# Optimization experiments

Measured on AMD Instinct MI355X. Metric: run time of the kernel, lower is better.

Reference implementation:

```python
import jax, jax.numpy as jnp
import numpy as np

B, S, D = 2, 2048, 2048
H, DK, DV, LD = 16, 128, 128, 64


def setup_inputs() -> dict:
    key = jax.random.key(0)
    ks = jax.random.split(key, 12)
    s = lambda fan_in: 1.0 / np.sqrt(fan_in)
    return {
        "queries": jax.random.normal(ks[0], (B, S, D), jnp.float32),
        "keys": jax.random.normal(ks[1], (B, S, D), jnp.float32),
        "values": jax.random.normal(ks[2], (B, S, D), jnp.float32),
        # linear_q: Linear(D, DK*H)
        "Wq": jax.random.uniform(ks[3], (D, DK * H), jnp.float32, -s(D), s(D)),
        "bq": jax.random.uniform(ks[4], (DK * H,), jnp.float32, -s(D), s(D)),
        # latent_k_proj / latent_v_proj: Linear(D, LD*H)
        "Wlk": jax.random.uniform(ks[5], (D, LD * H), jnp.float32, -s(D), s(D)),
        "blk": jax.random.uniform(ks[6], (LD * H,), jnp.float32, -s(D), s(D)),
        "Wlv": jax.random.uniform(ks[7], (D, LD * H), jnp.float32, -s(D), s(D)),
        "blv": jax.random.uniform(ks[8], (LD * H,), jnp.float32, -s(D), s(D)),
        # k/v reconstruction: Linear(LD, DK/DV, bias=False), stored [LD, DK]
        "Wkr": jax.random.uniform(ks[9], (LD, DK), jnp.float32, -s(LD), s(LD)),
        "Wvr": jax.random.uniform(ks[10], (LD, DV), jnp.float32, -s(LD), s(LD)),
        # linear_out: Linear(DV*H, D)
        "Wout": jax.random.uniform(ks[11], (DV * H, D), jnp.float32, -s(DV * H), s(DV * H)),
        "bout": jnp.zeros((D,), jnp.float32),
    }


def reference(queries, keys, values, Wq, bq, Wlk, blk, Wlv, blv, Wkr, Wvr, Wout, bout):
    b, sq, _ = queries.shape
    sk = keys.shape[1]
    # Q projection -> [b, H, sq, DK]
    q = (queries @ Wq + bq).reshape(b, sq, H, DK).transpose(0, 2, 1, 3)
    # Low-rank latent K/V -> [b, H, sk, LD]
    lk = (keys @ Wlk + blk).reshape(b, sk, H, LD).transpose(0, 2, 1, 3)
    lv = (values @ Wlv + blv).reshape(b, sk, H, LD).transpose(0, 2, 1, 3)
    # Reconstruct full K/V from latents -> [b, H, sk, DK/DV]
    k = lk @ Wkr
    v = lv @ Wvr
    scores = jnp.einsum('bhqd,bhkd->bhqk', q, k) / np.sqrt(DK).astype(np.float32)
    causal = jnp.triu(jnp.ones((sq, sk), dtype=bool), k=1)
    scores = jnp.where(causal, -jnp.inf, scores)
    attn = jax.nn.softmax(scores, axis=-1)
    out = jnp.einsum('bhqk,bhkd->bhqd', attn, v)  # [b, H, sq, DV]
    out = out.transpose(0, 2, 1, 3).reshape(b, sq, H * DV)
    return out @ Wout + bout
```

## Files before the change

kernel.cpp:

```cpp
#include <hip/hip_runtime.h>

#define S_LEN 2048
#define NH 16

typedef unsigned short u16;
typedef __attribute__((ext_vector_type(8))) short bf16x8;
typedef __attribute__((ext_vector_type(4))) short s16x4;
typedef __attribute__((ext_vector_type(4))) unsigned short u16x4;
typedef __attribute__((ext_vector_type(4))) unsigned int u32x4;
typedef __attribute__((ext_vector_type(4))) float f32x4;

__device__ __forceinline__ u16 f2bf(float f) {
  union { float f; unsigned int i; } x; x.f = f;
  unsigned int r = x.i + 0x7FFFu + ((x.i >> 16) & 1u);
  return (u16)(r >> 16);
}
__device__ __forceinline__ unsigned pk2(float lo, float hi) {
  unsigned r;
  asm("v_cvt_pk_bf16_f32 %0, %1, %2" : "=v"(r) : "v"(lo), "v"(hi));
  return r;
}
__device__ __forceinline__ void glds16(const void* g, void* l) {
  __builtin_amdgcn_global_load_lds((const __attribute__((address_space(1))) void*)g,
                                   (__attribute__((address_space(3))) void*)l, 16, 0, 0);
}

__global__ __launch_bounds__(256) void cast_f32_bf16(const float* __restrict__ in,
                                                     u16* __restrict__ out) {
  size_t i = ((size_t)blockIdx.x * 256 + threadIdx.x) * 8;
  f32x4 a = *(const f32x4*)&in[i];
  f32x4 b = *(const f32x4*)&in[i + 4];
  u32x4 o;
  o[0] = pk2(a[0], a[1]);
  o[1] = pk2(a[2], a[3]);
  o[2] = pk2(b[0], b[1]);
  o[3] = pk2(b[2], b[3]);
  *(u32x4*)&out[i] = o;
}

__global__ __launch_bounds__(256) void cast2_f32_bf16(const float* __restrict__ i0,
                                                      const float* __restrict__ i1,
                                                      u16* __restrict__ o0,
                                                      u16* __restrict__ o1) {
  const float* in = blockIdx.y ? i1 : i0;
  u16* out = blockIdx.y ? o1 : o0;
  size_t i = ((size_t)blockIdx.x * 256 + threadIdx.x) * 8;
  f32x4 a = *(const f32x4*)&in[i];
  f32x4 b = *(const f32x4*)&in[i + 4];
  u32x4 o;
  o[0] = pk2(a[0], a[1]);
  o[1] = pk2(a[2], a[3]);
  o[2] = pk2(b[0], b[1]);
  o[3] = pk2(b[2], b[3]);
  *(u32x4*)&out[i] = o;
}

__global__ __launch_bounds__(256) void transpose2_f32_bf16(const float* __restrict__ i0,
                                                           const float* __restrict__ i1,
                                                           u16* __restrict__ o0,
                                                           u16* __restrict__ o1,
                                                           int K, int N) {
  const float* in = blockIdx.z ? i1 : i0;
  u16* out = blockIdx.z ? o1 : o0;
  __shared__ u16 tile[64][72];
  int k0 = blockIdx.y * 64, n0 = blockIdx.x * 64;
  int t = threadIdx.x;
#pragma unroll
  for (int i = 0; i < 4; ++i) {
    int idx = i * 256 + t;
    int r = idx >> 4;
    int c4 = (idx & 15) << 2;
    f32x4 v = *(const f32x4*)&in[(size_t)(k0 + r) * N + n0 + c4];
#pragma unroll
    for (int j = 0; j < 4; ++j) tile[r][c4 + j] = f2bf(v[j]);
  }
  __syncthreads();
#pragma unroll
  for (int i = 0; i < 4; ++i) {
    int idx = i * 256 + t;
    int r = idx >> 4;
    int c4 = (idx & 15) << 2;
    u16x4 v;
    v[0] = tile[c4 + 0][r];
    v[1] = tile[c4 + 1][r];
    v[2] = tile[c4 + 2][r];
    v[3] = tile[c4 + 3][r];
    *(u16x4*)&out[(size_t)(n0 + r) * K + k0 + c4] = v;
  }
}

__global__ __launch_bounds__(256) void transpose_f32_bf16(const float* __restrict__ in,
                                                          u16* __restrict__ out,
                                                          int K, int N) {
  __shared__ u16 tile[64][72];
  int k0 = blockIdx.y * 64, n0 = blockIdx.x * 64;
  int t = threadIdx.x;
#pragma unroll
  for (int i = 0; i < 4; ++i) {
    int idx = i * 256 + t;
    int r = idx >> 4;
    int c4 = (idx & 15) << 2;
    f32x4 v = *(const f32x4*)&in[(size_t)(k0 + r) * N + n0 + c4];
#pragma unroll
    for (int j = 0; j < 4; ++j) tile[r][c4 + j] = f2bf(v[j]);
  }
  __syncthreads();
#pragma unroll
  for (int i = 0; i < 4; ++i) {
    int idx = i * 256 + t;
    int r = idx >> 4;
    int c4 = (idx & 15) << 2;
    u16x4 v;
    v[0] = tile[c4 + 0][r];
    v[1] = tile[c4 + 1][r];
    v[2] = tile[c4 + 2][r];
    v[3] = tile[c4 + 3][r];
    *(u16x4*)&out[(size_t)(n0 + r) * K + k0 + c4] = v;
  }
}

__global__ __launch_bounds__(256) void absorb_q(const u16* __restrict__ Wkr,
                                                const u16* __restrict__ Wqb,
                                                u16* __restrict__ Wq2T) {
  int kb = blockIdx.x, h = blockIdx.y;
  int t = threadIdx.x, w = t >> 6, lane = t & 63, lq = lane & 15, hi = lane >> 4;
  int k0 = kb * 128 + w * 32;
  f32x4 acc[4][2];
#pragma unroll
  for (int i = 0; i < 4; ++i)
#pragma unroll
    for (int j = 0; j < 2; ++j) acc[i][j] = (f32x4){0.f, 0.f, 0.f, 0.f};
#pragma unroll
  for (int kk = 0; kk < 4; ++kk) {
    bf16x8 a[4], bb[2];
#pragma unroll
    for (int fld = 0; fld < 4; ++fld)
      a[fld] = *(const bf16x8*)&Wkr[(fld * 16 + lq) * 128 + kk * 32 + hi * 8];
#pragma unroll
    for (int fk = 0; fk < 2; ++fk)
      bb[fk] = *(const bf16x8*)&Wqb[(size_t)(k0 + fk * 16 + lq) * 2048 + h * 128 + kk * 32 + hi * 8];
#pragma unroll
    for (int fld = 0; fld < 4; ++fld)
#pragma unroll
      for (int fk = 0; fk < 2; ++fk)
        acc[fld][fk] = __builtin_amdgcn_mfma_f32_16x16x32_bf16(a[fld], bb[fk], acc[fld][fk], 0, 0, 0);
  }
#pragma unroll
  for (int fld = 0; fld < 4; ++fld)
#pragma unroll
    for (int fk = 0; fk < 2; ++fk)
#pragma unroll
      for (int r = 0; r < 4; ++r)
        Wq2T[(size_t)(h * 64 + fld * 16 + hi * 4 + r) * 2048 + k0 + fk * 16 + lq] =
            f2bf(acc[fld][fk][r]);
}

__global__ __launch_bounds__(256) void absorb_o(const u16* __restrict__ WoutT,
                                                const u16* __restrict__ Wvr,
                                                u16* __restrict__ W2T) {
  int nb = blockIdx.x, h = blockIdx.y;
  int t = threadIdx.x, w = t >> 6, lane = t & 63, lq = lane & 15, hi = lane >> 4;
  int n0 = nb * 128 + w * 32;
  f32x4 acc[2][4];
#pragma unroll
  for (int i = 0; i < 2; ++i)
#pragma unroll
    for (int j = 0; j < 4; ++j) acc[i][j] = (f32x4){0.f, 0.f, 0.f, 0.f};
#pragma unroll
  for (int kk = 0; kk < 4; ++kk) {
    bf16x8 a[2], bb[4];
#pragma unroll
    for (int fn = 0; fn < 2; ++fn)
      a[fn] = *(const bf16x8*)&WoutT[(size_t)(n0 + fn * 16 + lq) * 2048 + h * 128 + kk * 32 + hi * 8];
#pragma unroll
    for (int fld = 0; fld < 4; ++fld)
      bb[fld] = *(const bf16x8*)&Wvr[(fld * 16 + lq) * 128 + kk * 32 + hi * 8];
#pragma unroll
    for (int fn = 0; fn < 2; ++fn)
#pragma unroll
      for (int fld = 0; fld < 4; ++fld)
        acc[fn][fld] = __builtin_amdgcn_mfma_f32_16x16x32_bf16(a[fn], bb[fld], acc[fn][fld], 0, 0, 0);
  }
#pragma unroll
  for (int fn = 0; fn < 2; ++fn)
#pragma unroll
    for (int fld = 0; fld < 4; ++fld)
#pragma unroll
      for (int r = 0; r < 4; ++r)
        W2T[(size_t)(n0 + fn * 16 + hi * 4 + r) * 1024 + h * 64 + fld * 16 + lq] =
            f2bf(acc[fn][fld][r]);
}

__global__ __launch_bounds__(256) void absorb_bq(const float* __restrict__ bq,
                                                 const float* __restrict__ Wkr,
                                                 float* __restrict__ bq2) {
  int n = blockIdx.x * 256 + threadIdx.x;
  int h = n >> 6, ld = n & 63;
  float s = 0.f;
#pragma unroll 8
  for (int dk = 0; dk < 128; ++dk) s += bq[h * 128 + dk] * Wkr[ld * 128 + dk];
  bq2[n] = s;
}

__global__ __launch_bounds__(256, 3) void gemm_projf(const float* __restrict__ A0,
                                                     const float* __restrict__ A1,
                                                     const float* __restrict__ A2,
                                                     const u16* __restrict__ W0,
                                                     const u16* __restrict__ W1,
                                                     const u16* __restrict__ W2,
                                                     const float* __restrict__ b0,
                                                     const float* __restrict__ b1,
                                                     const float* __restrict__ b2,
                                                     u16* __restrict__ C0,
                                                     u16* __restrict__ C1,
                                                     u16* __restrict__ C2) {
  const int N = 1024, K = 2048, nxl = 3, NT = 64;
  __shared__ u16 abuf[2][128 * 32];
  __shared__ u16 bbuf[3][128 * 32];

  int Lb = blockIdx.x;
  int xcd = Lb & 7, slot = Lb >> 3;
  int panel = ((slot >> nxl) << 3) + xcd;
  int x = slot & ((1 << nxl) - 1);
  int z = panel >> 5, y = panel & 31;

  const float* A = z == 0 ? A0 : (z == 1 ? A1 : A2);
  const u16* Wt = z == 0 ? W0 : (z == 1 ? W1 : W2);
  const float* bias = z == 0 ? b0 : (z == 1 ? b1 : b2);
  u16* C = z == 0 ? C0 : (z == 1 ? C1 : C2);

  int m0 = y * 128, n0 = x * 128;
  int t = threadIdx.x;
  int lane = t & 63, lq = lane & 15, hi = lane >> 4;
  int w = t >> 6, wm = w >> 1, wn = w & 1;

  struct a16 { f32x4 lo, hi; };
  a16 areg[2][2];

  f32x4 acc[4][4];
#pragma unroll
  for (int im = 0; im < 4; ++im)
#pragma unroll
    for (int fn = 0; fn < 4; ++fn) acc[im][fn] = (f32x4){0.f, 0.f, 0.f, 0.f};

#define LOADA(SLOT, KT)                                                              \
  do {                                                                               \
    int kb_ = (KT) * 32;                                                             \
    _Pragma("unroll") for (int i = 0; i < 2; ++i) {                                  \
      int idx = i * 256 + t, row = idx >> 2, c = idx & 3;                            \
      const float* ap = &A[(size_t)(m0 + row) * K + kb_ + ((c ^ ((row >> 1) & 3)) << 3)]; \
      areg[SLOT][i].lo = *(const f32x4*)ap;                                          \
      areg[SLOT][i].hi = *(const f32x4*)(ap + 4);                                    \
    }                                                                                \
  } while (0)

#define WRITEA(SLOT)                                                                 \
  do {                                                                               \
    _Pragma("unroll") for (int i = 0; i < 2; ++i) {                                  \
      u32x4 o;                                                                       \
      o[0] = pk2(areg[SLOT][i].lo[0], areg[SLOT][i].lo[1]);                          \
      o[1] = pk2(areg[SLOT][i].lo[2], areg[SLOT][i].lo[3]);                          \
      o[2] = pk2(areg[SLOT][i].hi[0], areg[SLOT][i].hi[1]);                          \
      o[3] = pk2(areg[SLOT][i].hi[2], areg[SLOT][i].hi[3]);                          \
      *(u32x4*)&abuf[SLOT][(i * 256 + t) * 8] = o;                                   \
    }                                                                                \
  } while (0)

#define STAGEB(KT)                                                                   \
  do {                                                                               \
    int kb_ = (KT) * 32;                                                             \
    u16* lB_ = &bbuf[(KT) % 3][0];                                                   \
    _Pragma("unroll") for (int i = 0; i < 2; ++i) {                                  \
      int idx = i * 256 + t, row = idx >> 2, c = idx & 3;                            \
      glds16(&Wt[(size_t)(n0 + row) * K + kb_ + ((c ^ ((row >> 1) & 3)) << 3)], lB_ + idx * 8); \
    }                                                                                \
  } while (0)

#define COMPUTE(PAR, TT)                                                             \
  do {                                                                               \
    const u16* lB_ = &bbuf[(TT) % 3][0];                                             \
    bf16x8 bf[4];                                                                    \
    _Pragma("unroll") for (int fn = 0; fn < 4; ++fn) {                               \
      int row = wn * 64 + fn * 16 + lq;                                              \
      bf[fn] = *(const bf16x8*)&lB_[row * 32 + ((hi ^ ((row >> 1) & 3)) << 3)];      \
    }                                                                                \
    __builtin_amdgcn_s_setprio(1);                                                   \
    _Pragma("unroll") for (int im = 0; im < 4; ++im) {                               \
      int row = wm * 64 + im * 16 + lq;                                              \
      bf16x8 af = *(const bf16x8*)&abuf[PAR][row * 32 + ((hi ^ ((row >> 1) & 3)) << 3)]; \
      _Pragma("unroll") for (int fn = 0; fn < 4; ++fn)                               \
        acc[im][fn] = __builtin_amdgcn_mfma_f32_16x16x32_bf16(af, bf[fn], acc[im][fn], 0, 0, 0); \
    }                                                                                \
    __builtin_amdgcn_s_setprio(0);                                                   \
  } while (0)

#define PSTEP(TT, PAR)                                                               \
  do {                                                                               \
    if ((TT) + 2 < NT) {                                                             \
      LOADA(PAR, (TT) + 2);                                                          \
      STAGEB((TT) + 2);                                                              \
    }                                                                                \
    COMPUTE(PAR, TT);                                                                \
    if ((TT) + 1 < NT) WRITEA(PAR ^ 1);         \
    if ((TT) + 2 < NT)                                                               \
      asm volatile("s_waitcnt vmcnt(6)" ::: "memory");                               \
    else                                                                             \
      asm volatile("s_waitcnt vmcnt(0)" ::: "memory");                               \
    asm volatile("s_waitcnt lgkmcnt(0)" ::: "memory");                               \
    __builtin_amdgcn_s_barrier();                                                    \
    __builtin_amdgcn_sched_barrier(0);                                               \
  } while (0)

  LOADA(0, 0);
  STAGEB(0);
  LOADA(1, 1);
  STAGEB(1);
  asm volatile("s_waitcnt vmcnt(8)" ::: "memory");
  WRITEA(0);
  asm volatile("s_waitcnt vmcnt(6)" ::: "memory");
  asm volatile("s_waitcnt lgkmcnt(0)" ::: "memory");
  __builtin_amdgcn_s_barrier();
  __builtin_amdgcn_sched_barrier(0);

  for (int tt = 0; tt < NT; tt += 2) {
    PSTEP(tt, 0);
    PSTEP(tt + 1, 1);
  }

#pragma unroll
  for (int im = 0; im < 4; ++im)
#pragma unroll
    for (int fn = 0; fn < 4; ++fn) {
      int col = n0 + wn * 64 + fn * 16 + lq;
      float bv = bias[col];
      int rbase = m0 + wm * 64 + im * 16 + hi * 4;
#pragma unroll
      for (int r = 0; r < 4; ++r)
        C[(size_t)(rbase + r) * N + col] = f2bf(acc[im][fn][r] + bv);
    }
#undef LOADA
#undef WRITEA
#undef STAGEB
#undef COMPUTE
#undef PSTEP
}

__global__ __launch_bounds__(256, 3) void gemm_dp(const u16* __restrict__ A,
                                                  const u16* __restrict__ Wt,
                                                  const float* __restrict__ bias,
                                                  float* __restrict__ Cv,
                                                  int N, int K, int nxl) {
  __shared__ u16 ldsA[3][128 * 32];
  __shared__ u16 ldsB[3][128 * 32];

  int Lb = blockIdx.x;
  int xcd = Lb & 7, slot = Lb >> 3;
  int panel = ((slot >> nxl) << 3) + xcd;
  int x = slot & ((1 << nxl) - 1);
  int y = panel & 31;

  int m0 = y * 128, n0 = x * 128;
  int t = threadIdx.x;
  int lane = t & 63, lq = lane & 15, hi = lane >> 4;
  int w = t >> 6, wm = w >> 1, wn = w & 1;
  int NT = K >> 5;

  auto stage = [&](int q, int kt) {
    u16* lA = &ldsA[q][0];
    u16* lB = &ldsB[q][0];
    int kb = kt * 32;
#pragma unroll
    for (int i = 0; i < 2; ++i) {
      int idx = i * 256 + t;
      int row = idx >> 2, c = idx & 3;
      glds16(&A[(size_t)(m0 + row) * K + kb + ((c ^ ((row >> 1) & 3)) << 3)], lA + idx * 8);
    }
#pragma unroll
    for (int i = 0; i < 2; ++i) {
      int idx = i * 256 + t;
      int row = idx >> 2, c = idx & 3;
      glds16(&Wt[(size_t)(n0 + row) * K + kb + ((c ^ ((row >> 1) & 3)) << 3)], lB + idx * 8);
    }
  };

  f32x4 acc[4][4];
#pragma unroll
  for (int im = 0; im < 4; ++im)
#pragma unroll
    for (int fn = 0; fn < 4; ++fn) acc[im][fn] = (f32x4){0.f, 0.f, 0.f, 0.f};

  stage(0, 0);
  stage(1, 1);
  asm volatile("s_waitcnt vmcnt(4)" ::: "memory");
  __builtin_amdgcn_s_barrier();

  for (int tt = 0; tt < NT; ++tt) {
    int q = tt % 3;
    if (tt + 2 < NT) stage((tt + 2) % 3, tt + 2);
    const u16* lA = &ldsA[q][0];
    const u16* lB = &ldsB[q][0];
    bf16x8 bf[4];
#pragma unroll
    for (int fn = 0; fn < 4; ++fn) {
      int row = wn * 64 + fn * 16 + lq;
      bf[fn] = *(const bf16x8*)&lB[row * 32 + ((hi ^ ((row >> 1) & 3)) << 3)];
    }
    __builtin_amdgcn_s_setprio(1);
#pragma unroll
    for (int im = 0; im < 4; ++im) {
      int row = wm * 64 + im * 16 + lq;
      bf16x8 af = *(const bf16x8*)&lA[row * 32 + ((hi ^ ((row >> 1) & 3)) << 3)];
#pragma unroll
      for (int fn = 0; fn < 4; ++fn)
        acc[im][fn] = __builtin_amdgcn_mfma_f32_16x16x32_bf16(af, bf[fn], acc[im][fn], 0, 0, 0);
    }
    __builtin_amdgcn_s_setprio(0);
    if (tt + 2 < NT)
      asm volatile("s_waitcnt vmcnt(4)" ::: "memory");
    else
      asm volatile("s_waitcnt vmcnt(0)" ::: "memory");
    __builtin_amdgcn_s_barrier();
  }

#pragma unroll
  for (int im = 0; im < 4; ++im)
#pragma unroll
    for (int fn = 0; fn < 4; ++fn) {
      int col = n0 + wn * 64 + fn * 16 + lq;
      float bv = bias[col];
      int rbase = m0 + wm * 64 + im * 16 + hi * 4;
#pragma unroll
      for (int r = 0; r < 4; ++r)
        Cv[(size_t)(rbase + r) * N + col] = acc[im][fn][r] + bv;
    }
}

__global__ __launch_bounds__(256) void transpose_lv(const u16* __restrict__ LV,
                                                    u16* __restrict__ out) {
  __shared__ u16 tile[64 * 72];
  int st = blockIdx.x, bh = blockIdx.y;
  int b = bh >> 4, h = bh & 15;
  int t = threadIdx.x;
  int s0 = st * 64;
#pragma unroll
  for (int i = 0; i < 2; ++i) {
    int idx = i * 256 + t;
    int sr = idx >> 3, c8 = idx & 7;
    bf16x8 v = *(const bf16x8*)&LV[(size_t)(b * S_LEN + s0 + sr) * 1024 + h * 64 + c8 * 8];
    int pos = (sr & 32) + ((sr & 12) << 1) + ((sr & 16) >> 2) + (sr & 3);
#pragma unroll
    for (int j = 0; j < 8; ++j) tile[(c8 * 8 + j) * 72 + pos] = (u16)v[j];
  }
  __syncthreads();
  u16* ob = out + (size_t)bh * 64 * S_LEN;
#pragma unroll
  for (int i = 0; i < 2; ++i) {
    int idx = i * 256 + t;
    int ld = idx >> 3, c8 = idx & 7;
    bf16x8 v = *(const bf16x8*)&tile[ld * 72 + c8 * 8];
    *(bf16x8*)&ob[(size_t)ld * S_LEN + s0 + c8 * 8] = v;
  }
}

__global__ __launch_bounds__(256) void mla_attn5(const u16* __restrict__ Qp,
                                                 const u16* __restrict__ LK,
                                                 const u16* __restrict__ LVt,
                                                 u16* __restrict__ O) {
  __shared__ u16 smem[16384];
  int Lb = blockIdx.x + blockIdx.y * 8;
  int half = Lb >> 9;
  int i0 = Lb & 511;
  int xcd = i0 & 7, ii = i0 >> 3;
  int bh = xcd * 4 + (ii & 3);
  int pr = ii >> 2;
  int qsup = half ? (31 - pr) : pr;
  int b = bh >> 4, h = bh & 15;
  int t = threadIdx.x, w = t >> 6, lane = t & 63, lq = lane & 15, hi = lane >> 4;
  int lq7 = lq & 7;

  const u16* Kb = LK + (size_t)b * S_LEN * 1024 + h * 64;
  const u16* Vb = LVt + (size_t)bh * 64 * S_LEN;
  const float scale = 0.08838834764831845f;

  auto stage = [&](int buf, int k0) {
    u16* lK = smem + buf * 4096;
    u16* lV = smem + 8192 + buf * 4096;
#pragma unroll
    for (int i = 0; i < 2; ++i) {
      int idx = i * 256 + t;
      int row = idx >> 3, c8 = idx & 7;
      glds16(Kb + (size_t)(k0 + row) * 1024 + ((c8 ^ (row & 7)) << 3), lK + idx * 8);
    }
#pragma unroll
    for (int i = 0; i < 2; ++i) {
      int idx = i * 256 + t;
      int row = idx >> 3, c8 = idx & 7;
      glds16(Vb + (size_t)row * S_LEN + k0 + ((c8 ^ (row & 7)) << 3), lV + idx * 8);
    }
  };

  int qb = qsup * 64;
  int nt = qsup + 1;
  int q0 = qb + w * 16;
  int kmax = q0 + 16;

  bf16x8 qf[2];
  {
    const u16* Qrow = Qp + (size_t)(b * S_LEN + q0 + lq) * 1024 + h * 64;
    qf[0] = *(const bf16x8*)&Qrow[hi * 8];
    qf[1] = *(const bf16x8*)&Qrow[32 + hi * 8];
  }

  f32x4 acc[4];
#pragma unroll
  for (int f = 0; f < 4; ++f) acc[f] = (f32x4){0.f, 0.f, 0.f, 0.f};
  float m = -1e30f, l = 0.f;

  stage(0, 0);
  __syncthreads();
  for (int tt = 0; tt < nt; ++tt) {
    int cur = tt & 1;
    if (tt + 1 < nt) stage(cur ^ 1, (tt + 1) * 64);
    int k0 = tt * 64;
    if (k0 < kmax) {
      const u16* lK = smem + cur * 4096;
      const u16* lV = smem + 8192 + cur * 4096;
      f32x4 sc[4];
#pragma unroll
      for (int kf = 0; kf < 4; ++kf) sc[kf] = (f32x4){0.f, 0.f, 0.f, 0.f};
      __builtin_amdgcn_s_setprio(1);
#pragma unroll
      for (int kf = 0; kf < 4; ++kf) {
        const u16* kr = lK + (kf * 16 + lq) * 64;
#pragma unroll
        for (int d0 = 0; d0 < 2; ++d0) {
          bf16x8 af = *(const bf16x8*)&kr[(((d0 << 2) + hi) ^ lq7) << 3];
          sc[kf] = __builtin_amdgcn_mfma_f32_16x16x32_bf16(af, qf[d0], sc[kf], 0, 0, 0);
        }
      }
      __builtin_amdgcn_s_setprio(0);
      int q = q0 + lq;
      float sv[16];
#pragma unroll
      for (int kf = 0; kf < 4; ++kf)
#pragma unroll
        for (int r = 0; r < 4; ++r) sv[kf * 4 + r] = sc[kf][r] * scale;
      if (k0 + 63 > q0) {
#pragma unroll
        for (int kf = 0; kf < 4; ++kf)
#pragma unroll
          for (int r = 0; r < 4; ++r)
            if (k0 + kf * 16 + hi * 4 + r > q) sv[kf * 4 + r] = -1e30f;
      }
      float tm = sv[0];
#pragma unroll
      for (int j = 1; j < 16; ++j) tm = fmaxf(tm, sv[j]);
      tm = fmaxf(tm, __shfl_xor(tm, 16));
      tm = fmaxf(tm, __shfl_xor(tm, 32));
      float p[16], ps = 0.f;
      if (__all(tm <= m + 8.f)) {
#pragma unroll
        for (int j = 0; j < 16; ++j) { p[j] = __expf(sv[j] - m); ps += p[j]; }
        ps += __shfl_xor(ps, 16);
        ps += __shfl_xor(ps, 32);
        l += ps;
      } else {
        float mnew = fmaxf(m, tm);
        float alpha = __expf(m - mnew);
#pragma unroll
        for (int j = 0; j < 16; ++j) { p[j] = __expf(sv[j] - mnew); ps += p[j]; }
        ps += __shfl_xor(ps, 16);
        ps += __shfl_xor(ps, 32);
        l = l * alpha + ps;
        m = mnew;
#pragma unroll
        for (int f = 0; f < 4; ++f) {
          acc[f][0] *= alpha; acc[f][1] *= alpha;
          acc[f][2] *= alpha; acc[f][3] *= alpha;
        }
      }
      bf16x8 pb[2];
#pragma unroll
      for (int ks = 0; ks < 2; ++ks) {
        union { u32x4 u; bf16x8 v; } pu;
#pragma unroll
        for (int wd = 0; wd < 4; ++wd) pu.u[wd] = pk2(p[ks * 8 + 2 * wd], p[ks * 8 + 2 * wd + 1]);
        pb[ks] = pu.v;
      }
      __builtin_amdgcn_s_setprio(1);
#pragma unroll
      for (int f = 0; f < 4; ++f) {
        const u16* vr = lV + (f * 16 + lq) * 64;
#pragma unroll
        for (int ks = 0; ks < 2; ++ks) {
          bf16x8 va = *(const bf16x8*)&vr[(((ks << 2) + hi) ^ lq7) << 3];
          acc[f] = __builtin_amdgcn_mfma_f32_16x16x32_bf16(va, pb[ks], acc[f], 0, 0, 0);
        }
      }
      __builtin_amdgcn_s_setprio(0);
    }
    __syncthreads();
  }
  {
    float inv = 1.f / l;
    int qloc = w * 16 + lq;
#pragma unroll
    for (int f = 0; f < 4; ++f)
#pragma unroll
      for (int r = 0; r < 4; ++r) {
        int col = f * 16 + hi * 4 + r;
        smem[qloc * 64 + (((col >> 3) ^ lq7) << 3) + (col & 7)] = f2bf(acc[f][r] * inv);
      }
  }
  __syncthreads();
#pragma unroll
  for (int i = 0; i < 2; ++i) {
    int cid = i * 256 + t;
    int q = cid >> 3, ch = cid & 7;
    bf16x8 v = *(const bf16x8*)&smem[q * 64 + ((ch ^ (q & 7)) << 3)];
    *(bf16x8*)&O[(size_t)(b * S_LEN + qb + q) * 1024 + h * 64 + (ch << 3)] = v;
  }
}

extern "C" void kernel_launch(void* const* d_in, const int* in_sizes, int n_in,
                              void* d_out, int out_size, void* d_ws, size_t ws_size,
                              hipStream_t stream) {
  const float* queries = (const float*)d_in[0];
  const float* keys    = (const float*)d_in[1];
  const float* values  = (const float*)d_in[2];
  const float* Wq      = (const float*)d_in[3];
  const float* bq      = (const float*)d_in[4];
  const float* Wlk     = (const float*)d_in[5];
  const float* blk     = (const float*)d_in[6];
  const float* Wlv     = (const float*)d_in[7];
  const float* blv     = (const float*)d_in[8];
  const float* Wkr     = (const float*)d_in[9];
  const float* Wvr     = (const float*)d_in[10];
  const float* Wout    = (const float*)d_in[11];
  const float* bout    = (const float*)d_in[12];

  u16* ws = (u16*)d_ws;
  u16* WqBf  = ws; ws += (size_t)2048 * 2048;
  u16* WkrBf = ws; ws += 64 * 128;
  u16* WvrBf = ws; ws += 64 * 128;
  u16* WoutT = ws; ws += (size_t)2048 * 2048;
  u16* WlkT  = ws; ws += (size_t)1024 * 2048;
  u16* WlvT  = ws; ws += (size_t)1024 * 2048;
  u16* Wq2T  = ws; ws += (size_t)1024 * 2048;
  u16* W2T   = ws; ws += (size_t)2048 * 1024;
  float* bq2 = (float*)ws; ws += 2048;
  u16* Qp    = ws; ws += (size_t)4096 * 1024;
  u16* LKb   = ws; ws += (size_t)4096 * 1024;
  u16* LVb   = ws; ws += (size_t)4096 * 1024;
  u16* LVt   = ws; ws += (size_t)32 * 64 * S_LEN;
  u16* Ob    = ws; ws += (size_t)4096 * 1024;

  dim3 blk256(256);
  cast_f32_bf16<<<dim3(2048), blk256, 0, stream>>>(Wq, WqBf);
  cast2_f32_bf16<<<dim3(4, 2), blk256, 0, stream>>>(Wkr, Wvr, WkrBf, WvrBf);

  transpose2_f32_bf16<<<dim3(16, 32, 2), blk256, 0, stream>>>(Wlk, Wlv, WlkT, WlvT, 2048, 1024);
  transpose_f32_bf16<<<dim3(32, 32), blk256, 0, stream>>>(Wout, WoutT, 2048, 2048);

  absorb_q<<<dim3(16, 16), blk256, 0, stream>>>(WkrBf, WqBf, Wq2T);
  absorb_o<<<dim3(16, 16), blk256, 0, stream>>>(WoutT, WvrBf, W2T);
  absorb_bq<<<dim3(4), blk256, 0, stream>>>(bq, Wkr, bq2);

  gemm_projf<<<dim3(768), blk256, 0, stream>>>(
      queries, keys, values, Wq2T, WlkT, WlvT, bq2, blk, blv, Qp, LKb, LVb);

  transpose_lv<<<dim3(32, 32), blk256, 0, stream>>>(LVb, LVt);

  mla_attn5<<<dim3(8, 128), blk256, 0, stream>>>(Qp, LKb, LVt, Ob);

  gemm_dp<<<dim3(512), blk256, 0, stream>>>(
      Ob, W2T, bout, (float*)d_out, 2048, 1024, 4);
}
```

Before: 183.1 us.

## Load fp32 A fragments directly into registers, bypassing LDS staging in projection GEMM

```diff
diff --git a/kernel.cpp b/kernel.cpp
--- a/kernel.cpp
+++ b/kernel.cpp
@@ -215,7 +215,6 @@
                                                      u16* __restrict__ C1,
                                                      u16* __restrict__ C2) {
   const int N = 1024, K = 2048, nxl = 3, NT = 64;
-  __shared__ u16 abuf[2][128 * 32];
   __shared__ u16 bbuf[3][128 * 32];
 
   int Lb = blockIdx.x;
@@ -234,35 +233,20 @@
   int lane = t & 63, lq = lane & 15, hi = lane >> 4;
   int w = t >> 6, wm = w >> 1, wn = w & 1;
 
-  struct a16 { f32x4 lo, hi; };
-  a16 areg[2][2];
-
+  f32x4 alo[4], ahi[4];
   f32x4 acc[4][4];
 #pragma unroll
   for (int im = 0; im < 4; ++im)
 #pragma unroll
     for (int fn = 0; fn < 4; ++fn) acc[im][fn] = (f32x4){0.f, 0.f, 0.f, 0.f};
 
-#define LOADA(SLOT, KT)                                                              \
+#define LOADA(KT)                                                                    \
   do {                                                                               \
     int kb_ = (KT) * 32;                                                             \
-    _Pragma("unroll") for (int i = 0; i < 2; ++i) {                                  \
-      int idx = i * 256 + t, row = idx >> 2, c = idx & 3;                            \
-      const float* ap = &A[(size_t)(m0 + row) * K + kb_ + ((c ^ ((row >> 1) & 3)) << 3)]; \
-      areg[SLOT][i].lo = *(const f32x4*)ap;                                          \
-      areg[SLOT][i].hi = *(const f32x4*)(ap + 4);                                    \
-    }                                                                                \
-  } while (0)
-
-#define WRITEA(SLOT)                                                                 \
-  do {                                                                               \
-    _Pragma("unroll") for (int i = 0; i < 2; ++i) {                                  \
-      u32x4 o;                                                                       \
-      o[0] = pk2(areg[SLOT][i].lo[0], areg[SLOT][i].lo[1]);                          \
-      o[1] = pk2(areg[SLOT][i].lo[2], areg[SLOT][i].lo[3]);                          \
-      o[2] = pk2(areg[SLOT][i].hi[0], areg[SLOT][i].hi[1]);                          \
-      o[3] = pk2(areg[SLOT][i].hi[2], areg[SLOT][i].hi[3]);                          \
-      *(u32x4*)&abuf[SLOT][(i * 256 + t) * 8] = o;                                   \
+    _Pragma("unroll") for (int im = 0; im < 4; ++im) {                               \
+      const float* ap = &A[(size_t)(m0 + wm * 64 + im * 16 + lq) * K + kb_ + hi * 8];\
+      alo[im] = *(const f32x4*)ap;                                                   \
+      ahi[im] = *(const f32x4*)(ap + 4);                                             \
     }                                                                                \
   } while (0)
 
@@ -276,55 +260,44 @@
     }                                                                                \
   } while (0)
 
-#define COMPUTE(PAR, TT)                                                             \
-  do {                                                                               \
-    const u16* lB_ = &bbuf[(TT) % 3][0];                                             \
-    bf16x8 bf[4];                                                                    \
-    _Pragma("unroll") for (int fn = 0; fn < 4; ++fn) {                               \
-      int row = wn * 64 + fn * 16 + lq;                                              \
-      bf[fn] = *(const bf16x8*)&lB_[row * 32 + ((hi ^ ((row >> 1) & 3)) << 3)];      \
-    }                                                                                \
-    __builtin_amdgcn_s_setprio(1);                                                   \
-    _Pragma("unroll") for (int im = 0; im < 4; ++im) {                               \
-      int row = wm * 64 + im * 16 + lq;                                              \
-      bf16x8 af = *(const bf16x8*)&abuf[PAR][row * 32 + ((hi ^ ((row >> 1) & 3)) << 3)]; \
-      _Pragma("unroll") for (int fn = 0; fn < 4; ++fn)                               \
-        acc[im][fn] = __builtin_amdgcn_mfma_f32_16x16x32_bf16(af, bf[fn], acc[im][fn], 0, 0, 0); \
-    }                                                                                \
-    __builtin_amdgcn_s_setprio(0);                                                   \
-  } while (0)
-
-#define PSTEP(TT, PAR)                                                               \
-  do {                                                                               \
-    if ((TT) + 2 < NT) {                                                             \
-      LOADA(PAR, (TT) + 2);                                                          \
-      STAGEB((TT) + 2);                                                              \
-    }                                                                                \
-    COMPUTE(PAR, TT);                                                                \
-    if ((TT) + 1 < NT) WRITEA(PAR ^ 1);         \
-    if ((TT) + 2 < NT)                                                               \
-      asm volatile("s_waitcnt vmcnt(6)" ::: "memory");                               \
-    else                                                                             \
-      asm volatile("s_waitcnt vmcnt(0)" ::: "memory");                               \
-    asm volatile("s_waitcnt lgkmcnt(0)" ::: "memory");                               \
-    __builtin_amdgcn_s_barrier();                                                    \
-    __builtin_amdgcn_sched_barrier(0);                                               \
-  } while (0)
-
-  LOADA(0, 0);
+  LOADA(0);
   STAGEB(0);
-  LOADA(1, 1);
   STAGEB(1);
-  asm volatile("s_waitcnt vmcnt(8)" ::: "memory");
-  WRITEA(0);
-  asm volatile("s_waitcnt vmcnt(6)" ::: "memory");
-  asm volatile("s_waitcnt lgkmcnt(0)" ::: "memory");
+  asm volatile("s_waitcnt vmcnt(2)" ::: "memory");
   __builtin_amdgcn_s_barrier();
-  __builtin_amdgcn_sched_barrier(0);
-
-  for (int tt = 0; tt < NT; tt += 2) {
-    PSTEP(tt, 0);
-    PSTEP(tt + 1, 1);
+
+  for (int tt = 0; tt < NT; ++tt) {
+    bf16x8 af[4];
+#pragma unroll
+    for (int im = 0; im < 4; ++im) {
+      union { u32x4 u; bf16x8 v; } pu;
+      pu.u[0] = pk2(alo[im][0], alo[im][1]);
+      pu.u[1] = pk2(alo[im][2], alo[im][3]);
+      pu.u[2] = pk2(ahi[im][0], ahi[im][1]);
+      pu.u[3] = pk2(ahi[im][2], ahi[im][3]);
+      af[im] = pu.v;
+    }
+    if (tt + 1 < NT) LOADA(tt + 1);
+    if (tt + 2 < NT) STAGEB(tt + 2);
+    const u16* lB_ = &bbuf[tt % 3][0];
+    bf16x8 bf[4];
+#pragma unroll
+    for (int fn = 0; fn < 4; ++fn) {
+      int row = wn * 64 + fn * 16 + lq;
+      bf[fn] = *(const bf16x8*)&lB_[row * 32 + ((hi ^ ((row >> 1) & 3)) << 3)];
+    }
+    __builtin_amdgcn_s_setprio(1);
+#pragma unroll
+    for (int im = 0; im < 4; ++im)
+#pragma unroll
+      for (int fn = 0; fn < 4; ++fn)
+        acc[im][fn] = __builtin_amdgcn_mfma_f32_16x16x32_bf16(af[im], bf[fn], acc[im][fn], 0, 0, 0);
+    __builtin_amdgcn_s_setprio(0);
+    if (tt + 2 < NT)
+      asm volatile("s_waitcnt vmcnt(10)" ::: "memory");
+    else if (tt + 1 < NT)
+      asm volatile("s_waitcnt vmcnt(8)" ::: "memory");
+    __builtin_amdgcn_s_barrier();
   }
 
 #pragma unroll
@@ -339,10 +312,7 @@
         C[(size_t)(rbase + r) * N + col] = f2bf(acc[im][fn][r] + bv);
     }
 #undef LOADA
-#undef WRITEA
 #undef STAGEB
-#undef COMPUTE
-#undef PSTEP
 }
 
 __global__ __launch_bounds__(256, 3) void gemm_dp(const u16* __restrict__ A,
```

Result: slower. 301.3 us (+64.5%).

## Load fp32 A operand directly into MFMA registers, bypassing LDS staging

Applied to the files above, without the earlier changes.

```diff
diff --git a/kernel.cpp b/kernel.cpp
--- a/kernel.cpp
+++ b/kernel.cpp
@@ -215,7 +215,6 @@
                                                      u16* __restrict__ C1,
                                                      u16* __restrict__ C2) {
   const int N = 1024, K = 2048, nxl = 3, NT = 64;
-  __shared__ u16 abuf[2][128 * 32];
   __shared__ u16 bbuf[3][128 * 32];
 
   int Lb = blockIdx.x;
@@ -234,9 +233,7 @@
   int lane = t & 63, lq = lane & 15, hi = lane >> 4;
   int w = t >> 6, wm = w >> 1, wn = w & 1;
 
-  struct a16 { f32x4 lo, hi; };
-  a16 areg[2][2];
-
+  f32x4 alo[2][4], ahi[2][4];
   f32x4 acc[4][4];
 #pragma unroll
   for (int im = 0; im < 4; ++im)
@@ -246,23 +243,10 @@
 #define LOADA(SLOT, KT)                                                              \
   do {                                                                               \
     int kb_ = (KT) * 32;                                                             \
-    _Pragma("unroll") for (int i = 0; i < 2; ++i) {                                  \
-      int idx = i * 256 + t, row = idx >> 2, c = idx & 3;                            \
-      const float* ap = &A[(size_t)(m0 + row) * K + kb_ + ((c ^ ((row >> 1) & 3)) << 3)]; \
-      areg[SLOT][i].lo = *(const f32x4*)ap;                                          \
-      areg[SLOT][i].hi = *(const f32x4*)(ap + 4);                                    \
-    }                                                                                \
-  } while (0)
-
-#define WRITEA(SLOT)                                                                 \
-  do {                                                                               \
-    _Pragma("unroll") for (int i = 0; i < 2; ++i) {                                  \
-      u32x4 o;                                                                       \
-      o[0] = pk2(areg[SLOT][i].lo[0], areg[SLOT][i].lo[1]);                          \
-      o[1] = pk2(areg[SLOT][i].lo[2], areg[SLOT][i].lo[3]);                          \
-      o[2] = pk2(areg[SLOT][i].hi[0], areg[SLOT][i].hi[1]);                          \
-      o[3] = pk2(areg[SLOT][i].hi[2], areg[SLOT][i].hi[3]);                          \
-      *(u32x4*)&abuf[SLOT][(i * 256 + t) * 8] = o;                                   \
+    _Pragma("unroll") for (int im = 0; im < 4; ++im) {                               \
+      const float* ap = &A[(size_t)(m0 + wm * 64 + im * 16 + lq) * K + kb_ + hi * 8];\
+      alo[SLOT][im] = *(const f32x4*)ap;                                             \
+      ahi[SLOT][im] = *(const f32x4*)(ap + 4);                                       \
     }                                                                                \
   } while (0)
 
@@ -276,8 +260,21 @@
     }                                                                                \
   } while (0)
 
-#define COMPUTE(PAR, TT)                                                             \
+#define PHASE(TT, PAR)                                                               \
   do {                                                                               \
+    bf16x8 af[4];                                                                    \
+    _Pragma("unroll") for (int im = 0; im < 4; ++im) {                               \
+      union { u32x4 u; bf16x8 v; } pu;                                               \
+      pu.u[0] = pk2(alo[PAR][im][0], alo[PAR][im][1]);                               \
+      pu.u[1] = pk2(alo[PAR][im][2], alo[PAR][im][3]);                               \
+      pu.u[2] = pk2(ahi[PAR][im][0], ahi[PAR][im][1]);                               \
+      pu.u[3] = pk2(ahi[PAR][im][2], ahi[PAR][im][3]);                               \
+      af[im] = pu.v;                                                                 \
+    }                                                                                \
+    if ((TT) + 2 < NT) {                                                             \
+      LOADA(PAR, (TT) + 2);                                                          \
+      STAGEB((TT) + 2);                                                              \
+    }                                                                                \
     const u16* lB_ = &bbuf[(TT) % 3][0];                                             \
     bf16x8 bf[4];                                                                    \
     _Pragma("unroll") for (int fn = 0; fn < 4; ++fn) {                               \
@@ -285,46 +282,27 @@
       bf[fn] = *(const bf16x8*)&lB_[row * 32 + ((hi ^ ((row >> 1) & 3)) << 3)];      \
     }                                                                                \
     __builtin_amdgcn_s_setprio(1);                                                   \
-    _Pragma("unroll") for (int im = 0; im < 4; ++im) {                               \
-      int row = wm * 64 + im * 16 + lq;                                              \
-      bf16x8 af = *(const bf16x8*)&abuf[PAR][row * 32 + ((hi ^ ((row >> 1) & 3)) << 3)]; \
+    _Pragma("unroll") for (int im = 0; im < 4; ++im)                                 \
       _Pragma("unroll") for (int fn = 0; fn < 4; ++fn)                               \
-        acc[im][fn] = __builtin_amdgcn_mfma_f32_16x16x32_bf16(af, bf[fn], acc[im][fn], 0, 0, 0); \
-    }                                                                                \
+        acc[im][fn] = __builtin_amdgcn_mfma_f32_16x16x32_bf16(af[im], bf[fn], acc[im][fn], 0, 0, 0); \
     __builtin_amdgcn_s_setprio(0);                                                   \
-  } while (0)
-
-#define PSTEP(TT, PAR)                                                               \
-  do {                                                                               \
-    if ((TT) + 2 < NT) {                                                             \
-      LOADA(PAR, (TT) + 2);                                                          \
-      STAGEB((TT) + 2);                                                              \
-    }                                                                                \
-    COMPUTE(PAR, TT);                                                                \
-    if ((TT) + 1 < NT) WRITEA(PAR ^ 1);         \
     if ((TT) + 2 < NT)                                                               \
-      asm volatile("s_waitcnt vmcnt(6)" ::: "memory");                               \
-    else                                                                             \
-      asm volatile("s_waitcnt vmcnt(0)" ::: "memory");                               \
-    asm volatile("s_waitcnt lgkmcnt(0)" ::: "memory");                               \
+      asm volatile("s_waitcnt vmcnt(10)" ::: "memory");   \
+    else if ((TT) + 1 < NT)                                                          \
+      asm volatile("s_waitcnt vmcnt(0)" ::: "memory");               \
     __builtin_amdgcn_s_barrier();                                                    \
-    __builtin_amdgcn_sched_barrier(0);                                               \
   } while (0)
 
   LOADA(0, 0);
   STAGEB(0);
   LOADA(1, 1);
   STAGEB(1);
-  asm volatile("s_waitcnt vmcnt(8)" ::: "memory");
-  WRITEA(0);
-  asm volatile("s_waitcnt vmcnt(6)" ::: "memory");
-  asm volatile("s_waitcnt lgkmcnt(0)" ::: "memory");
+  asm volatile("s_waitcnt vmcnt(10)" ::: "memory");
   __builtin_amdgcn_s_barrier();
-  __builtin_amdgcn_sched_barrier(0);
 
   for (int tt = 0; tt < NT; tt += 2) {
-    PSTEP(tt, 0);
-    PSTEP(tt + 1, 1);
+    PHASE(tt, 0);
+    PHASE(tt + 1, 1);
   }
 
 #pragma unroll
@@ -339,10 +317,8 @@
         C[(size_t)(rbase + r) * N + col] = f2bf(acc[im][fn][r] + bv);
     }
 #undef LOADA
-#undef WRITEA
 #undef STAGEB
-#undef COMPUTE
-#undef PSTEP
+#undef PHASE
 }
 
 __global__ __launch_bounds__(256, 3) void gemm_dp(const u16* __restrict__ A,
```

New measurement: 381.0 us. 108% more time.
